# Optimization experiments

Measured on AMD Instinct MI355X. Metric: run time of the kernel, lower is better.

## Reference

```python
import jax, jax.numpy as jnp
import numpy as np
from jax import lax

STEPS = 200
LR = 0.01
BATCH = 16384
PROJ = 8
HID = 64


def setup_inputs() -> dict:
    key = jax.random.key(0)
    k_spec, k_w1, k_w2, k_r = jax.random.split(key, 4)
    spectrum = jax.random.normal(k_spec, (BATCH, 40), dtype=jnp.float32)
    # forward_model params: MLP 6 -> 64 (tanh) -> 40
    W1 = jax.random.normal(k_w1, (6, HID), dtype=jnp.float32) * 0.3
    b1 = jnp.zeros((HID,), dtype=jnp.float32)
    W2 = jax.random.normal(k_w2, (HID, 40), dtype=jnp.float32) * 0.3
    b2 = jnp.zeros((40,), dtype=jnp.float32)
    # random projection, row-normalized (as in __init__)
    R = jax.random.normal(k_r, (PROJ, 40), dtype=jnp.float32)
    R = R / jnp.linalg.norm(R, axis=1, keepdims=True)
    return {"spectrum": spectrum, "W1": W1, "b1": b1, "W2": W2, "b2": b2, "R": R}


def reference(spectrum, W1, b1, W2, b2, R):
    def fwd_model(u):  # (6,) -> (40,)
        return jnp.tanh(u @ W1 + b1) @ W2 + b2

    def solve(spec):  # spec: (40,) -> u: (6,)
        def step(u, _):
            g_pred = fwd_model(u)
            error = g_pred - spec               # (40,)
            z = R @ error                       # (PROJ,)
            grad_est = R.T @ z                  # (40,)
            u = u - LR * grad_est[:6]
            u = jnp.clip(u, 0.0, 1.0)           # clamp=True
            return u, None

        u0 = jnp.full((6,), 0.5, dtype=spec.dtype)
        u_final, _ = lax.scan(step, u0, None, length=STEPS)
        return u_final

    return jax.vmap(solve)(spectrum)  # (BATCH, 6)
```

## Files before the change

kernel.cpp:

```cpp
#include <hip/hip_runtime.h>


static constexpr float LR_ = 0.01f;

typedef float v2f __attribute__((ext_vector_type(2)));

template <int CTRL>
__device__ __forceinline__ float dppx(float x) {
    return __int_as_float(
        __builtin_amdgcn_mov_dpp(__float_as_int(x), CTRL, 0xF, 0xF, true));
}
__device__ __forceinline__ void pin2(v2f& x) { asm volatile("" : "+v"(x)); }

__global__ __launch_bounds__(256)
__attribute__((amdgpu_waves_per_eu(2, 2)))
void solve_k(
    const float* __restrict__ spec, const float* __restrict__ W1,
    const float* __restrict__ b1,   const float* __restrict__ W2,
    const float* __restrict__ b2,   const float* __restrict__ R,
    float* __restrict__ out, int batch)
{
    __shared__ float sQs[64 * 7];
    __shared__ float sSs[240];

    const int t = threadIdx.x;

    if (t < 64) {
        float M[8];
        #pragma unroll
        for (int p = 0; p < 8; ++p) {
            float acc = 0.f;
            for (int k = 0; k < 40; ++k) acc = fmaf(W2[t*40+k], R[p*40+k], acc);
            M[p] = acc;
        }
        #pragma unroll
        for (int j = 0; j < 6; ++j) {
            float acc = 0.f;
            #pragma unroll
            for (int p = 0; p < 8; ++p) acc = fmaf(M[p], R[p*40+j], acc);
            sQs[t*7+j] = -LR_ * acc;
        }
    } else {
        for (int idx = t - 64; idx < 240; idx += 192) {
            int j = idx / 40, k = idx % 40;
            float acc = 0.f;
            #pragma unroll
            for (int p = 0; p < 8; ++p) acc = fmaf(R[p*40+j], R[p*40+k], acc);
            sSs[idx] = -LR_ * acc;
        }
    }
    __syncthreads();

    const int tid = blockIdx.x * 256 + t;
    const int s   = tid >> 3;
    const int sub = tid & 7;
    const int ib  = sub * 8;
    const bool live = (s < batch);
    const int sl = live ? s : 0;

    const float K = 2.8853900817779268f;

    v2f w1kp[6][4], b1kp[4];
    #pragma unroll
    for (int j = 0; j < 6; ++j)
        #pragma unroll
        for (int ip = 0; ip < 4; ++ip) {
            w1kp[j][ip].x = K * W1[j*64 + ib + 2*ip];
            w1kp[j][ip].y = K * W1[j*64 + ib + 2*ip + 1];
        }
    #pragma unroll
    for (int ip = 0; ip < 4; ++ip) {
        b1kp[ip].x = K * b1[ib + 2*ip];
        b1kp[ip].y = K * b1[ib + 2*ip + 1];
    }

    v2f qs2p[8][3];
    float qc[6];
    #pragma unroll
    for (int j = 0; j < 6; ++j) qc[j] = 0.f;
    #pragma unroll
    for (int i = 0; i < 8; ++i)
        #pragma unroll
        for (int m = 0; m < 3; ++m) {
            float a = sQs[(ib + i)*7 + 2*m];
            float b = sQs[(ib + i)*7 + 2*m + 1];
            qs2p[i][m].x = -2.f * a;
            qs2p[i][m].y = -2.f * b;
            qc[2*m]   += a;
            qc[2*m+1] += b;
        }

    float es[6];
    #pragma unroll
    for (int j = 0; j < 6; ++j) es[j] = 0.f;
    const float* sp = spec + sl * 40;
    for (int k = 0; k < 40; ++k) {
        float v = b2[k] - sp[k];
        #pragma unroll
        for (int j = 0; j < 6; ++j) es[j] = fmaf(v, sSs[j*40+k], es[j]);
    }
    v2f c2[3];
    #pragma unroll
    for (int m = 0; m < 3; ++m) {
        c2[m].x = es[2*m]   * 0.125f + qc[2*m];
        c2[m].y = es[2*m+1] * 0.125f + qc[2*m+1];
    }

    #pragma unroll
    for (int j = 0; j < 6; ++j)
        #pragma unroll
        for (int ip = 0; ip < 4; ++ip) pin2(w1kp[j][ip]);
    #pragma unroll
    for (int ip = 0; ip < 4; ++ip) pin2(b1kp[ip]);
    #pragma unroll
    for (int i = 0; i < 8; ++i)
        #pragma unroll
        for (int m = 0; m < 3; ++m) pin2(qs2p[i][m]);
    #pragma unroll
    for (int m = 0; m < 3; ++m) pin2(c2[m]);

    float u[6];
    #pragma unroll
    for (int j = 0; j < 6; ++j) u[j] = 0.5f;

    for (int step = 0; step < 200; ++step) {
        float r[8];
        #pragma unroll
        for (int ip = 0; ip < 4; ++ip) {
            v2f tt = b1kp[ip];
            #pragma unroll
            for (int j = 0; j < 6; ++j) {
                v2f ub = {u[j], u[j]};
                tt = __builtin_elementwise_fma(ub, w1kp[j][ip], tt);
            }
            v2f e1;
            e1.x = __builtin_amdgcn_exp2f(tt.x);
            e1.y = __builtin_amdgcn_exp2f(tt.y);
            e1 += (v2f){1.f, 1.f};
            r[2*ip]   = __builtin_amdgcn_rcpf(e1.x);
            r[2*ip+1] = __builtin_amdgcn_rcpf(e1.y);
        }
        v2f g2[3];
        #pragma unroll
        for (int m = 0; m < 3; ++m) {
            v2f up = {u[2*m], u[2*m+1]};
            g2[m] = __builtin_elementwise_fma(up, (v2f){0.125f, 0.125f}, c2[m]);
        }
        #pragma unroll
        for (int i = 0; i < 8; ++i) {
            v2f hb = {r[i], r[i]};
            #pragma unroll
            for (int m = 0; m < 3; ++m)
                g2[m] = __builtin_elementwise_fma(hb, qs2p[i][m], g2[m]);
        }
        #pragma unroll
        for (int m = 0; m < 3; ++m) {
            float ga = g2[m].x, gb = g2[m].y;
            ga += dppx<0xB1>(ga);   gb += dppx<0xB1>(gb);
            ga += dppx<0x4E>(ga);   gb += dppx<0x4E>(gb);
            ga += dppx<0x141>(ga);  gb += dppx<0x141>(gb);
            u[2*m]   = __builtin_amdgcn_fmed3f(ga, 0.f, 1.f);
            u[2*m+1] = __builtin_amdgcn_fmed3f(gb, 0.f, 1.f);
        }
    }

    if (live && sub == 0) {
        float* o = out + s * 6;
        #pragma unroll
        for (int j = 0; j < 6; ++j) o[j] = u[j];
    }
}

extern "C" void kernel_launch(void* const* d_in, const int* in_sizes, int n_in,
                              void* d_out, int out_size, void* d_ws, size_t ws_size,
                              hipStream_t stream)
{
    const float* spec = (const float*)d_in[0];
    const float* W1   = (const float*)d_in[1];
    const float* b1   = (const float*)d_in[2];
    const float* W2   = (const float*)d_in[3];
    const float* b2   = (const float*)d_in[4];
    const float* R    = (const float*)d_in[5];
    int batch = in_sizes[0] / 40;

    int threads = batch * 8;
    int blocks  = (threads + 255) / 256;
    hipLaunchKernelGGL(solve_k, dim3(blocks), dim3(256), 0, stream,
                       spec, W1, b1, W2, b2, R, (float*)d_out, batch);
}
```

Measured before the change: 153.2 us.

## Move hidden-to-gradient projection onto bf16x3-split MFMA with 16 samples per wave

Restructures the per-step update so each wave handles 16 samples. The 64-wide hidden activations are split into three bf16 parts and multiplied against a similarly split projection matrix with 16x16x32 bf16 MFMAs, replacing the packed-FMA plus DPP reduction. Updated u values are redistributed through LDS each step, and occupancy is pinned to one wave per EU. This cuts VALU work and the thread count per sample, at the cost of bf16-split accuracy, extra conversion work, LDS round-trips each step, and lower occupancy.

```diff
diff --git a/kernel.cpp b/kernel.cpp
--- a/kernel.cpp
+++ b/kernel.cpp
@@ -3,17 +3,46 @@
 
 static constexpr float LR_ = 0.01f;
 
-typedef float v2f __attribute__((ext_vector_type(2)));
-
-template <int CTRL>
-__device__ __forceinline__ float dppx(float x) {
-    return __int_as_float(
-        __builtin_amdgcn_mov_dpp(__float_as_int(x), CTRL, 0xF, 0xF, true));
-}
-__device__ __forceinline__ void pin2(v2f& x) { asm volatile("" : "+v"(x)); }
+typedef float v2f   __attribute__((ext_vector_type(2)));
+typedef float f32x4 __attribute__((ext_vector_type(4)));
+typedef int   i32x4 __attribute__((ext_vector_type(4)));
+typedef short s16x8 __attribute__((ext_vector_type(8)));
+
+__device__ __forceinline__ void pin2(v2f& x)   { asm volatile("" : "+v"(x)); }
+__device__ __forceinline__ void pin4(i32x4& x) { asm volatile("" : "+v"(x)); }
+__device__ __forceinline__ void pinf4(f32x4& x){ asm volatile("" : "+v"(x)); }
+
+#define PK_FMA_LO(T, U, W)                                                   \
+    asm("v_pk_fma_f32 %0, %1, %2, %0 op_sel:[0,0,0] op_sel_hi:[0,1,1]"       \
+        : "+v"(T) : "v"(U), "v"(W))
+#define PK_FMA_HI(T, U, W)                                                   \
+    asm("v_pk_fma_f32 %0, %1, %2, %0 op_sel:[1,0,0] op_sel_hi:[1,1,1]"       \
+        : "+v"(T) : "v"(U), "v"(W))
+
+__device__ __forceinline__ unsigned cvt_pk_bf16(float lo, float hi) {
+    unsigned d;
+    asm("v_cvt_pk_bf16_f32 %0, %1, %2" : "=v"(d) : "v"(lo), "v"(hi));
+    return d;
+}
+__device__ __forceinline__ float lo16f(unsigned p) {
+    return __int_as_float((int)(p << 16));
+}
+__device__ __forceinline__ float hi16f(unsigned p) {
+    return __int_as_float((int)(p & 0xffff0000u));
+}
+__device__ __forceinline__ void split3(float x, float y,
+                                       unsigned& p1, unsigned& p2, unsigned& p3) {
+    p1 = cvt_pk_bf16(x, y);
+    float dx = x - lo16f(p1), dy = y - hi16f(p1);
+    p2 = cvt_pk_bf16(dx, dy);
+    p3 = cvt_pk_bf16(dx - lo16f(p2), dy - hi16f(p2));
+}
+__device__ __forceinline__ s16x8 mk8(unsigned a, unsigned b, unsigned c, unsigned d) {
+    return __builtin_bit_cast(s16x8, (i32x4){(int)a, (int)b, (int)c, (int)d});
+}
 
 __global__ __launch_bounds__(256)
-__attribute__((amdgpu_waves_per_eu(2, 2)))
+__attribute__((amdgpu_waves_per_eu(1, 1)))
 void solve_k(
     const float* __restrict__ spec, const float* __restrict__ W1,
     const float* __restrict__ b1,   const float* __restrict__ W2,
@@ -22,6 +51,7 @@
 {
     __shared__ float sQs[64 * 7];
     __shared__ float sSs[240];
+    __shared__ __attribute__((aligned(16))) float sUT[4][6][16];
 
     const int t = threadIdx.x;
 
@@ -51,123 +81,170 @@
     }
     __syncthreads();
 
-    const int tid = blockIdx.x * 256 + t;
-    const int s   = tid >> 3;
-    const int sub = tid & 7;
-    const int ib  = sub * 8;
-    const bool live = (s < batch);
-    const int sl = live ? s : 0;
+    const int w     = t >> 6;
+    const int l     = t & 63;
+    const int col   = l & 15;
+    const int grp   = l >> 4;
+    const int sbase = blockIdx.x * 64 + w * 16;
 
     const float K = 2.8853900817779268f;
 
-    v2f w1kp[6][4], b1kp[4];
+    v2f w1kp[6][2][4], b1kp[2][4];
     #pragma unroll
     for (int j = 0; j < 6; ++j)
         #pragma unroll
-        for (int ip = 0; ip < 4; ++ip) {
-            w1kp[j][ip].x = K * W1[j*64 + ib + 2*ip];
-            w1kp[j][ip].y = K * W1[j*64 + ib + 2*ip + 1];
-        }
-    #pragma unroll
-    for (int ip = 0; ip < 4; ++ip) {
-        b1kp[ip].x = K * b1[ib + 2*ip];
-        b1kp[ip].y = K * b1[ib + 2*ip + 1];
-    }
-
-    v2f qs2p[8][3];
-    float qc[6];
-    #pragma unroll
-    for (int j = 0; j < 6; ++j) qc[j] = 0.f;
-    #pragma unroll
-    for (int i = 0; i < 8; ++i)
-        #pragma unroll
-        for (int m = 0; m < 3; ++m) {
-            float a = sQs[(ib + i)*7 + 2*m];
-            float b = sQs[(ib + i)*7 + 2*m + 1];
-            qs2p[i][m].x = -2.f * a;
-            qs2p[i][m].y = -2.f * b;
-            qc[2*m]   += a;
-            qc[2*m+1] += b;
-        }
-
-    float es[6];
-    #pragma unroll
-    for (int j = 0; j < 6; ++j) es[j] = 0.f;
-    const float* sp = spec + sl * 40;
-    for (int k = 0; k < 40; ++k) {
-        float v = b2[k] - sp[k];
-        #pragma unroll
-        for (int j = 0; j < 6; ++j) es[j] = fmaf(v, sSs[j*40+k], es[j]);
-    }
-    v2f c2[3];
-    #pragma unroll
-    for (int m = 0; m < 3; ++m) {
-        c2[m].x = es[2*m]   * 0.125f + qc[2*m];
-        c2[m].y = es[2*m+1] * 0.125f + qc[2*m+1];
-    }
+        for (int tile = 0; tile < 2; ++tile)
+            #pragma unroll
+            for (int rp = 0; rp < 4; ++rp) {
+                int uu = 32*tile + grp*8 + 2*rp;
+                w1kp[j][tile][rp].x = K * W1[j*64 + uu];
+                w1kp[j][tile][rp].y = K * W1[j*64 + uu + 1];
+            }
+    #pragma unroll
+    for (int tile = 0; tile < 2; ++tile)
+        #pragma unroll
+        for (int rp = 0; rp < 4; ++rp) {
+            int uu = 32*tile + grp*8 + 2*rp;
+            b1kp[tile][rp].x = K * b1[uu];
+            b1kp[tile][rp].y = K * b1[uu + 1];
+        }
+
+    i32x4 B1W[2], B2W[2], B3W[2];
+    #pragma unroll
+    for (int tile = 0; tile < 2; ++tile) {
+        unsigned w1_[4], w2_[4], w3_[4];
+        #pragma unroll
+        for (int rp = 0; rp < 4; ++rp) {
+            int uu = 32*tile + grp*8 + 2*rp;
+            float q0 = 0.f, q1 = 0.f;
+            if (col < 6) {
+                q0 = -2.f * sQs[uu*7 + col];
+                q1 = -2.f * sQs[(uu+1)*7 + col];
+            }
+            split3(q0, q1, w1_[rp], w2_[rp], w3_[rp]);
+        }
+        B1W[tile] = (i32x4){(int)w1_[0], (int)w1_[1], (int)w1_[2], (int)w1_[3]};
+        B2W[tile] = (i32x4){(int)w2_[0], (int)w2_[1], (int)w2_[2], (int)w2_[3]};
+        B3W[tile] = (i32x4){(int)w3_[0], (int)w3_[1], (int)w3_[2], (int)w3_[3]};
+    }
+
+    float esD[4] = {0.f, 0.f, 0.f, 0.f};
+    if (col < 6) {
+        float qcol = 0.f;
+        for (int i = 0; i < 64; ++i) qcol += sQs[i*7 + col];
+        #pragma unroll
+        for (int q = 0; q < 4; ++q) {
+            int srow = sbase + grp*4 + q;
+            int sl2 = srow < batch ? srow : 0;
+            const float* sp = spec + sl2 * 40;
+            float acc = qcol;
+            for (int k = 0; k < 40; ++k)
+                acc = fmaf(b2[k] - sp[k], sSs[col*40 + k], acc);
+            esD[q] = acc;
+        }
+    }
+
+    f32x4 uD = (col < 6) ? (f32x4){0.5f, 0.5f, 0.5f, 0.5f}
+                         : (f32x4){0.f, 0.f, 0.f, 0.f};
+    f32x4 esD4 = {esD[0], esD[1], esD[2], esD[3]};
+
+    v2f u2[3];
+    u2[0] = u2[1] = u2[2] = (v2f){0.5f, 0.5f};
 
     #pragma unroll
     for (int j = 0; j < 6; ++j)
         #pragma unroll
-        for (int ip = 0; ip < 4; ++ip) pin2(w1kp[j][ip]);
-    #pragma unroll
-    for (int ip = 0; ip < 4; ++ip) pin2(b1kp[ip]);
-    #pragma unroll
-    for (int i = 0; i < 8; ++i)
-        #pragma unroll
-        for (int m = 0; m < 3; ++m) pin2(qs2p[i][m]);
-    #pragma unroll
-    for (int m = 0; m < 3; ++m) pin2(c2[m]);
-
-    float u[6];
-    #pragma unroll
-    for (int j = 0; j < 6; ++j) u[j] = 0.5f;
+        for (int tile = 0; tile < 2; ++tile)
+            #pragma unroll
+            for (int rp = 0; rp < 4; ++rp) pin2(w1kp[j][tile][rp]);
+    #pragma unroll
+    for (int tile = 0; tile < 2; ++tile)
+        #pragma unroll
+        for (int rp = 0; rp < 4; ++rp) pin2(b1kp[tile][rp]);
+    pin4(B1W[0]); pin4(B1W[1]); pin4(B2W[0]); pin4(B2W[1]);
+    pin4(B3W[0]); pin4(B3W[1]); pinf4(esD4);
+
+    const s16x8 B1_0 = __builtin_bit_cast(s16x8, B1W[0]);
+    const s16x8 B1_1 = __builtin_bit_cast(s16x8, B1W[1]);
+    const s16x8 B2_0 = __builtin_bit_cast(s16x8, B2W[0]);
+    const s16x8 B2_1 = __builtin_bit_cast(s16x8, B2W[1]);
+    const s16x8 B3_0 = __builtin_bit_cast(s16x8, B3W[0]);
+    const s16x8 B3_1 = __builtin_bit_cast(s16x8, B3W[1]);
+    const f32x4 zero4 = {0.f, 0.f, 0.f, 0.f};
 
     for (int step = 0; step < 200; ++step) {
-        float r[8];
-        #pragma unroll
-        for (int ip = 0; ip < 4; ++ip) {
-            v2f tt = b1kp[ip];
-            #pragma unroll
-            for (int j = 0; j < 6; ++j) {
-                v2f ub = {u[j], u[j]};
-                tt = __builtin_elementwise_fma(ub, w1kp[j][ip], tt);
+        v2f tt[2][4];
+        #pragma unroll
+        for (int tile = 0; tile < 2; ++tile)
+            #pragma unroll
+            for (int rp = 0; rp < 4; ++rp) tt[tile][rp] = b1kp[tile][rp];
+        #pragma unroll
+        for (int jp = 0; jp < 3; ++jp) {
+            #pragma unroll
+            for (int tile = 0; tile < 2; ++tile)
+                #pragma unroll
+                for (int rp = 0; rp < 4; ++rp)
+                    PK_FMA_LO(tt[tile][rp], u2[jp], w1kp[2*jp][tile][rp]);
+            #pragma unroll
+            for (int tile = 0; tile < 2; ++tile)
+                #pragma unroll
+                for (int rp = 0; rp < 4; ++rp)
+                    PK_FMA_HI(tt[tile][rp], u2[jp], w1kp[2*jp+1][tile][rp]);
+        }
+        unsigned a1[2][4], a2[2][4], a3[2][4];
+        #pragma unroll
+        for (int tile = 0; tile < 2; ++tile)
+            #pragma unroll
+            for (int rp = 0; rp < 4; ++rp) {
+                v2f e;
+                e.x = __builtin_amdgcn_exp2f(tt[tile][rp].x);
+                e.y = __builtin_amdgcn_exp2f(tt[tile][rp].y);
+                e += (v2f){1.f, 1.f};
+                float rx = __builtin_amdgcn_rcpf(e.x);
+                float ry = __builtin_amdgcn_rcpf(e.y);
+                split3(rx, ry, a1[tile][rp], a2[tile][rp], a3[tile][rp]);
             }
-            v2f e1;
-            e1.x = __builtin_amdgcn_exp2f(tt.x);
-            e1.y = __builtin_amdgcn_exp2f(tt.y);
-            e1 += (v2f){1.f, 1.f};
-            r[2*ip]   = __builtin_amdgcn_rcpf(e1.x);
-            r[2*ip+1] = __builtin_amdgcn_rcpf(e1.y);
-        }
-        v2f g2[3];
-        #pragma unroll
-        for (int m = 0; m < 3; ++m) {
-            v2f up = {u[2*m], u[2*m+1]};
-            g2[m] = __builtin_elementwise_fma(up, (v2f){0.125f, 0.125f}, c2[m]);
-        }
-        #pragma unroll
-        for (int i = 0; i < 8; ++i) {
-            v2f hb = {r[i], r[i]};
-            #pragma unroll
-            for (int m = 0; m < 3; ++m)
-                g2[m] = __builtin_elementwise_fma(hb, qs2p[i][m], g2[m]);
-        }
-        #pragma unroll
-        for (int m = 0; m < 3; ++m) {
-            float ga = g2[m].x, gb = g2[m].y;
-            ga += dppx<0xB1>(ga);   gb += dppx<0xB1>(gb);
-            ga += dppx<0x4E>(ga);   gb += dppx<0x4E>(gb);
-            ga += dppx<0x141>(ga);  gb += dppx<0x141>(gb);
-            u[2*m]   = __builtin_amdgcn_fmed3f(ga, 0.f, 1.f);
-            u[2*m+1] = __builtin_amdgcn_fmed3f(gb, 0.f, 1.f);
-        }
-    }
-
-    if (live && sub == 0) {
-        float* o = out + s * 6;
-        #pragma unroll
-        for (int j = 0; j < 6; ++j) o[j] = u[j];
+        s16x8 A1_0 = mk8(a1[0][0], a1[0][1], a1[0][2], a1[0][3]);
+        s16x8 A2_0 = mk8(a2[0][0], a2[0][1], a2[0][2], a2[0][3]);
+        s16x8 A3_0 = mk8(a3[0][0], a3[0][1], a3[0][2], a3[0][3]);
+        s16x8 A1_1 = mk8(a1[1][0], a1[1][1], a1[1][2], a1[1][3]);
+        s16x8 A2_1 = mk8(a2[1][0], a2[1][1], a2[1][2], a2[1][3]);
+        s16x8 A3_1 = mk8(a3[1][0], a3[1][1], a3[1][2], a3[1][3]);
+
+        f32x4 C = uD + esD4;
+        f32x4 c00 = __builtin_amdgcn_mfma_f32_16x16x32_bf16(A1_0, B1_0, C, 0, 0, 0);
+        c00 = __builtin_amdgcn_mfma_f32_16x16x32_bf16(A2_0, B1_0, c00, 0, 0, 0);
+        c00 = __builtin_amdgcn_mfma_f32_16x16x32_bf16(A3_0, B1_0, c00, 0, 0, 0);
+        f32x4 c01 = __builtin_amdgcn_mfma_f32_16x16x32_bf16(A1_0, B2_0, zero4, 0, 0, 0);
+        c01 = __builtin_amdgcn_mfma_f32_16x16x32_bf16(A2_0, B2_0, c01, 0, 0, 0);
+        c01 = __builtin_amdgcn_mfma_f32_16x16x32_bf16(A1_0, B3_0, c01, 0, 0, 0);
+        f32x4 c10 = __builtin_amdgcn_mfma_f32_16x16x32_bf16(A1_1, B1_1, zero4, 0, 0, 0);
+        c10 = __builtin_amdgcn_mfma_f32_16x16x32_bf16(A2_1, B1_1, c10, 0, 0, 0);
+        c10 = __builtin_amdgcn_mfma_f32_16x16x32_bf16(A3_1, B1_1, c10, 0, 0, 0);
+        f32x4 c11 = __builtin_amdgcn_mfma_f32_16x16x32_bf16(A1_1, B2_1, zero4, 0, 0, 0);
+        c11 = __builtin_amdgcn_mfma_f32_16x16x32_bf16(A2_1, B2_1, c11, 0, 0, 0);
+        c11 = __builtin_amdgcn_mfma_f32_16x16x32_bf16(A1_1, B3_1, c11, 0, 0, 0);
+        f32x4 D = (c00 + c01) + (c10 + c11);
+        #pragma unroll
+        for (int q = 0; q < 4; ++q)
+            uD[q] = __builtin_amdgcn_fmed3f(D[q], 0.f, 1.f);
+
+        if (col < 6)
+            *(f32x4*)&sUT[w][col][grp*4] = uD;
+        u2[0].x = sUT[w][0][col]; u2[0].y = sUT[w][1][col];
+        u2[1].x = sUT[w][2][col]; u2[1].y = sUT[w][3][col];
+        u2[2].x = sUT[w][4][col]; u2[2].y = sUT[w][5][col];
+    }
+
+    #pragma unroll
+    for (int it = 0; it < 2; ++it) {
+        int idx = l + 64*it;
+        if (idx < 96) {
+            int srow = idx / 6;
+            int j = idx - srow*6;
+            int gs = sbase + srow;
+            if (gs < batch) out[gs*6 + j] = sUT[w][j][srow];
+        }
     }
 }
 
@@ -183,7 +260,7 @@
     const float* R    = (const float*)d_in[5];
     int batch = in_sizes[0] / 40;
 
-    int threads = batch * 8;
+    int threads = batch * 4;
     int blocks  = (threads + 255) / 256;
     hipLaunchKernelGGL(solve_k, dim3(blocks), dim3(256), 0, stream,
                        spec, W1, b1, W2, b2, R, (float*)d_out, batch);
```

Result: slower. 196.5 us (+28.3%).
